# Optimization experiments

Hardware: AMD Instinct MI355X
Metric: run time of the kernel (lower is better)

The kernel has to match this reference:

```python
import jax, jax.numpy as jnp
import numpy as np

B, T, SD, DD = 256, 365, 64, 16
H, NH, L, FF = 256, 8, 4, 1024
K, P, N = 5, 30, 10000
DEG = np.pi / 180.0


def _ln(x, g, b):
    mu = x.mean(-1, keepdims=True)
    var = ((x - mu) ** 2).mean(-1, keepdims=True)
    return g * (x - mu) / jnp.sqrt(var + 1e-5) + b


def _gelu(x):
    return jax.nn.gelu(x, approximate=False)


def _forward(static, dynamic, lat, lon, all_statics, station_coords,
             W_st, b_st, g_st, be_st, W_dy, b_dy, g_dy, be_dy,
             Wqkv, bqkv, Wo, bo, g_ln1, be_ln1, Wf1, bf1, Wf2, bf2, g_ln2, be_ln2,
             W_o1, b_o1, W_o2, b_o2, scale, shift):
    # denormalize to CONUS degrees, then radians (as BallTree haversine expects)
    lat_o = (lat + 1.0) / 2.0 * (49.0 - 24.0) + 24.0
    lon_o = (lon + 1.0) / 2.0 * (-66.5 + 125.0) - 125.0
    qlat = lat_o[:, 0] * DEG
    qlon = lon_o[:, 0] * DEG
    slat = station_coords[:, 0]
    slon = station_coords[:, 1]
    dlat = qlat[:, None] - slat[None, :]
    dlon = qlon[:, None] - slon[None, :]
    # haversine term; true distance = 2*asin(sqrt(hav)) is monotone in hav,
    # so ranking by hav reproduces BallTree(metric='haversine') neighbor order
    hav = jnp.sin(dlat / 2) ** 2 + jnp.cos(qlat)[:, None] * jnp.cos(slat)[None, :] * jnp.sin(dlon / 2) ** 2
    _, nbr = jax.lax.top_k(-hav, K + 1)          # [B, K+1] nearest stations
    nbr = nbr[:, 1:]                              # drop self (nearest), keep K
    neigh = all_statics[nbr].reshape(static.shape[0], K * SD)  # gather + flatten
    combined = jnp.concatenate([static, neigh], axis=-1)       # [B, (K+1)*SD]

    sfeat = _gelu(_ln(combined @ W_st + b_st, g_st, be_st))    # static_net (dropout=eval)
    x = _gelu(_ln(dynamic @ W_dy + b_dy, g_dy, be_dy)) + sfeat[:, None, :]

    hd = H // NH
    inv_sqrt_d = 1.0 / jnp.sqrt(jnp.float32(hd))
    Bq, Tq = x.shape[0], x.shape[1]
    for l in range(L):  # post-norm TransformerEncoderLayer, relu FF
        qkv = x @ Wqkv[l] + bqkv[l]
        q, k, v = jnp.split(qkv, 3, axis=-1)
        q = q.reshape(Bq, Tq, NH, hd)
        k = k.reshape(Bq, Tq, NH, hd)
        v = v.reshape(Bq, Tq, NH, hd)
        att = jax.nn.softmax(jnp.einsum('bqhd,bkhd->bhqk', q, k) * inv_sqrt_d, axis=-1)
        ao = jnp.einsum('bhqk,bkhd->bqhd', att, v).reshape(Bq, Tq, H) @ Wo[l] + bo[l]
        x = _ln(x + ao, g_ln1[l], be_ln1[l])
        ff = jax.nn.relu(x @ Wf1[l] + bf1[l]) @ Wf2[l] + bf2[l]
        x = _ln(x + ff, g_ln2[l], be_ln2[l])

    pooled = x.mean(axis=1)
    raw = jnp.tanh(_gelu((pooled + sfeat) @ W_o1 + b_o1) @ W_o2 + b_o2)
    return raw * scale + shift


def setup_inputs() -> dict:
    key = jax.random.key(0)
    ks = jax.random.split(key, 24)
    rn = lambda k, shp: jax.random.normal(k, shp, jnp.float32) * 0.02
    inp = {}
    inp['static'] = jax.random.normal(ks[0], (B, SD), jnp.float32)
    inp['dynamic'] = jax.random.normal(ks[1], (B, T, DD), jnp.float32)
    inp['lat'] = jax.random.uniform(ks[2], (B, 1), jnp.float32, -1.0, 1.0)
    inp['lon'] = jax.random.uniform(ks[3], (B, 1), jnp.float32, -1.0, 1.0)
    inp['all_statics'] = jax.random.normal(ks[4], (N, SD), jnp.float32)
    slat = jax.random.uniform(ks[5], (N,), jnp.float32, 24.0, 49.0) * DEG
    slon = jax.random.uniform(ks[6], (N,), jnp.float32, -125.0, -66.5) * DEG
    inp['station_coords'] = jnp.stack([slat, slon], axis=-1)
    # static_net
    inp['W_st'] = rn(ks[7], (SD * (K + 1), H)); inp['b_st'] = jnp.zeros(H)
    inp['g_st'] = jnp.ones(H); inp['be_st'] = jnp.zeros(H)
    # dynamic_emb
    inp['W_dy'] = rn(ks[8], (DD, H)); inp['b_dy'] = jnp.zeros(H)
    inp['g_dy'] = jnp.ones(H); inp['be_dy'] = jnp.zeros(H)
    # transformer (stacked over layers)
    inp['Wqkv'] = rn(ks[9], (L, H, 3 * H)); inp['bqkv'] = jnp.zeros((L, 3 * H))
    inp['Wo'] = rn(ks[10], (L, H, H)); inp['bo'] = jnp.zeros((L, H))
    inp['g_ln1'] = jnp.ones((L, H)); inp['be_ln1'] = jnp.zeros((L, H))
    inp['Wf1'] = rn(ks[11], (L, H, FF)); inp['bf1'] = jnp.zeros((L, FF))
    inp['Wf2'] = rn(ks[12], (L, FF, H)); inp['bf2'] = jnp.zeros((L, H))
    inp['g_ln2'] = jnp.ones((L, H)); inp['be_ln2'] = jnp.zeros((L, H))
    # output head
    inp['W_o1'] = rn(ks[13], (H, H // 2)); inp['b_o1'] = jnp.zeros(H // 2)
    inp['W_o2'] = rn(ks[14], (H // 2, P)); inp['b_o2'] = jnp.zeros(P)
    inp['scale'] = jnp.array(1.0, jnp.float32)
    inp['shift'] = jnp.array(0.0, jnp.float32)
    return inp


def reference(static, dynamic, lat, lon, all_statics, station_coords,
              W_st, b_st, g_st, be_st, W_dy, b_dy, g_dy, be_dy,
              Wqkv, bqkv, Wo, bo, g_ln1, be_ln1, Wf1, bf1, Wf2, bf2, g_ln2, be_ln2,
              W_o1, b_o1, W_o2, b_o2, scale, shift):
    return _forward(static, dynamic, lat, lon, all_statics, station_coords,
                    W_st, b_st, g_st, be_st, W_dy, b_dy, g_dy, be_dy,
                    Wqkv, bqkv, Wo, bo, g_ln1, be_ln1, Wf1, bf1, Wf2, bf2, g_ln2, be_ln2,
                    W_o1, b_o1, W_o2, b_o2, scale, shift)
```

## Files before the change

kernel.cpp:

```cpp
#include <hip/hip_runtime.h>
#include <math.h>

#define T_SEQ 365
#define HDIM 256
#define NHEADS 8
#define HD 32
#define BATCH 256
#define DDIM 16
#define FFDIM 1024
#define NST 10000
#define KNB 5
#define SDIM 64

typedef __bf16 bf16x8 __attribute__((ext_vector_type(8)));
typedef float  f32x16 __attribute__((ext_vector_type(16)));
typedef unsigned short u16x8 __attribute__((ext_vector_type(8)));

__device__ __forceinline__ ushort f2b_hi(float v) {
    unsigned u = __float_as_uint(v);
    unsigned r = u + 0x7fffu + ((u >> 16) & 1u);
    return (ushort)(r >> 16);
}
__device__ __forceinline__ float b2f(ushort h) {
    return __uint_as_float(((unsigned)h) << 16);
}
__device__ __forceinline__ ushort f2b_lo(float v, ushort hi) {
    return f2b_hi(v - b2f(hi));
}

__device__ __forceinline__ float gelu_f(float x) {
    return 0.5f * x * (1.f + erff(x * 0.70710678118654752f));
}


__device__ __forceinline__ float block_sum256(float v, float* sred) {
    #pragma unroll
    for (int off = 32; off; off >>= 1) v += __shfl_xor(v, off);
    int wave = threadIdx.x >> 6;
    if ((threadIdx.x & 63) == 0) sred[wave] = v;
    __syncthreads();
    float s = sred[0] + sred[1] + sred[2] + sred[3];
    __syncthreads();
    return s;
}

__global__ __launch_bounds__(256) void topk_kernel(
    const float* __restrict__ lat, const float* __restrict__ lon,
    const float* __restrict__ coords, int* __restrict__ nbr)
{
    __shared__ float hav[NST];
    __shared__ float rv[256];
    __shared__ int   ri[256];
    const float DEG = 0.017453292519943295f;
    int b = blockIdx.x, t = threadIdx.x;
    float lat_o = (lat[b] + 1.f) * 0.5f * 25.f + 24.f;
    float lon_o = (lon[b] + 1.f) * 0.5f * 58.5f - 125.f;
    float qlat = lat_o * DEG, qlon = lon_o * DEG;
    float cq = cosf(qlat);
    for (int i = t; i < NST; i += 256) {
        float slat = coords[2*i], slon = coords[2*i+1];
        float dlat = qlat - slat, dlon = qlon - slon;
        float s1 = sinf(dlat * 0.5f), s2 = sinf(dlon * 0.5f);
        hav[i] = s1*s1 + cq * cosf(slat) * s2*s2;
    }
    __syncthreads();
    for (int sel = 0; sel < KNB + 1; ++sel) {
        float bv = 1e30f; int bi = 0x7fffffff;
        for (int i = t; i < NST; i += 256) {
            float v = hav[i];
            if (v < bv || (v == bv && i < bi)) { bv = v; bi = i; }
        }
        rv[t] = bv; ri[t] = bi;
        __syncthreads();
        for (int s = 128; s > 0; s >>= 1) {
            if (t < s) {
                float ov = rv[t+s]; int oi = ri[t+s];
                if (ov < rv[t] || (ov == rv[t] && oi < ri[t])) { rv[t] = ov; ri[t] = oi; }
            }
            __syncthreads();
        }
        if (t == 0) {
            if (sel > 0) nbr[b*KNB + sel - 1] = ri[0];
            hav[ri[0]] = 1e30f;
        }
        __syncthreads();
    }
}

__global__ __launch_bounds__(256) void sfeat_kernel(
    const float* __restrict__ stat, const float* __restrict__ all_st,
    const int* __restrict__ nbr, const float* __restrict__ W,
    const float* __restrict__ bias, const float* __restrict__ g,
    const float* __restrict__ be, float* __restrict__ sfeat)
{
    __shared__ float comb[(KNB+1)*SDIM];
    __shared__ float sred[4];
    int b = blockIdx.x, t = threadIdx.x;
    for (int i = t; i < (KNB+1)*SDIM; i += 256) {
        if (i < SDIM) comb[i] = stat[b*SDIM + i];
        else {
            int n = (i - SDIM) >> 6, d = (i - SDIM) & 63;
            comb[i] = all_st[(size_t)nbr[b*KNB + n] * SDIM + d];
        }
    }
    __syncthreads();
    float acc = bias[t];
    for (int j = 0; j < (KNB+1)*SDIM; ++j)
        acc = fmaf(comb[j], W[j*HDIM + t], acc);
    float mu  = block_sum256(acc, sred) * (1.f/256.f);
    float d   = acc - mu;
    float var = block_sum256(d*d, sred) * (1.f/256.f);
    float y = g[t] * d * rsqrtf(var + 1e-5f) + be[t];
    sfeat[(size_t)b*HDIM + t] = gelu_f(y);
}

__global__ __launch_bounds__(256) void dyn_kernel(
    const float* __restrict__ dynv, const float* __restrict__ W,
    const float* __restrict__ bias, const float* __restrict__ g,
    const float* __restrict__ be, const float* __restrict__ sfeatc,
    ushort* __restrict__ xhi, ushort* __restrict__ xlo)
{
    __shared__ float w[DDIM*HDIM];
    __shared__ float dr[4][DDIM];
    int wave = threadIdx.x >> 6, lane = threadIdx.x & 63;
    int row0 = blockIdx.x * 4;
    for (int i = threadIdx.x; i < DDIM*HDIM; i += 256) w[i] = W[i];
    if (lane < DDIM)
        dr[wave][lane] = dynv[(size_t)(row0 + wave)*DDIM + lane];
    __syncthreads();
    int row = row0 + wave;
    int b = row / T_SEQ;
    int c0 = lane * 4;
    float v0 = bias[c0], v1 = bias[c0+1], v2 = bias[c0+2], v3 = bias[c0+3];
    #pragma unroll
    for (int k = 0; k < DDIM; ++k) {
        float dk = dr[wave][k];
        float4 wv = *reinterpret_cast<const float4*>(&w[k*HDIM + c0]);
        v0 = fmaf(dk, wv.x, v0); v1 = fmaf(dk, wv.y, v1);
        v2 = fmaf(dk, wv.z, v2); v3 = fmaf(dk, wv.w, v3);
    }
    float s = v0 + v1 + v2 + v3;
    #pragma unroll
    for (int off = 32; off; off >>= 1) s += __shfl_xor(s, off);
    float mu = s * (1.f/256.f);
    float d0 = v0-mu, d1 = v1-mu, d2 = v2-mu, d3 = v3-mu;
    float s2 = d0*d0 + d1*d1 + d2*d2 + d3*d3;
    #pragma unroll
    for (int off = 32; off; off >>= 1) s2 += __shfl_xor(s2, off);
    float rs = rsqrtf(s2 * (1.f/256.f) + 1e-5f);
    float4 gg = *reinterpret_cast<const float4*>(&g[c0]);
    float4 bb = *reinterpret_cast<const float4*>(&be[c0]);
    float4 sf = *reinterpret_cast<const float4*>(&sfeatc[(size_t)b*HDIM + c0]);
    float o0 = gelu_f(gg.x*d0*rs + bb.x) + sf.x;
    float o1 = gelu_f(gg.y*d1*rs + bb.y) + sf.y;
    float o2 = gelu_f(gg.z*d2*rs + bb.z) + sf.z;
    float o3 = gelu_f(gg.w*d3*rs + bb.w) + sf.w;
    size_t o = ((size_t)(row >> 5) * 32 + (c0 >> 3)) * 256 + ((row & 31) << 3) + (c0 & 7);
    ushort4 hv, lv;
    hv.x = f2b_hi(o0); lv.x = f2b_lo(o0, hv.x);
    hv.y = f2b_hi(o1); lv.y = f2b_lo(o1, hv.y);
    hv.z = f2b_hi(o2); lv.z = f2b_lo(o2, hv.z);
    hv.w = f2b_hi(o3); lv.w = f2b_lo(o3, hv.w);
    *reinterpret_cast<ushort4*>(&xhi[o]) = hv;
    *reinterpret_cast<ushort4*>(&xlo[o]) = lv;
}

__global__ __launch_bounds__(256) void tsplit_kernel(
    const float* __restrict__ W, ushort* __restrict__ hi, ushort* __restrict__ lo,
    int K, int N)
{
    __shared__ float tile[32][33];
    size_t l = blockIdx.z;
    const float* Wl = W + l*(size_t)K*N;
    ushort* hil = hi + l*(size_t)K*N;
    ushort* lol = lo + l*(size_t)K*N;
    int n0 = blockIdx.x*32, k0 = blockIdx.y*32;
    int tx = threadIdx.x & 31, ty = threadIdx.x >> 5;
    int KB = K >> 3;
    for (int i = ty; i < 32; i += 8) tile[i][tx] = Wl[(size_t)(k0+i)*N + n0 + tx];
    __syncthreads();
    for (int i = ty; i < 32; i += 8) {
        float v = tile[tx][i];
        ushort h = f2b_hi(v);
        size_t o = ((size_t)(n0 >> 5) * KB + (k0 >> 3) + (tx >> 3)) * 256
                 + ((size_t)i << 3) + (tx & 7);
        hil[o] = h;
        lol[o] = f2b_lo(v, h);
    }
}

template<int DO_RELU, int OUT>
__global__ __launch_bounds__(256) void gemm_mfma(
    const ushort* __restrict__ Ahi, const ushort* __restrict__ Alo,
    const ushort* __restrict__ Bhi, const ushort* __restrict__ Blo,
    const float* __restrict__ bias,
    ushort* __restrict__ Chi, ushort* __restrict__ Clo,
    ushort* __restrict__ Wq_h, ushort* __restrict__ Wq_l,
    ushort* __restrict__ Wk_h, ushort* __restrict__ Wk_l,
    ushort* __restrict__ Wv_h, ushort* __restrict__ Wv_l,
    int M, int N, int K)
{
    const int t = threadIdx.x;
    const int lane = t & 63, wave = t >> 6;
    const int wr = wave >> 1, wc = wave & 1;
    const int lr = lane & 31, kg = lane >> 5;
    const int row_b = blockIdx.y * 128 + wr * 64;
    const int col_b = blockIdx.x * 128 + wc * 64;
    const int KB = K >> 3;

    const ushort *pAh[2], *pAl[2], *pBh[2], *pBl[2];
    #pragma unroll
    for (int mi = 0; mi < 2; ++mi) {
        int rb = row_b + mi*32; if (rb > M - 32) rb = M - 32;
        size_t base = ((size_t)(rb >> 5) * KB + kg) * 256 + lr * 8;
        pAh[mi] = Ahi + base; pAl[mi] = Alo + base;
    }
    #pragma unroll
    for (int nj = 0; nj < 2; ++nj) {
        size_t base = ((size_t)((col_b + nj*32) >> 5) * KB + kg) * 256 + lr * 8;
        pBh[nj] = Bhi + base; pBl[nj] = Blo + base;
    }

    f32x16 acc[2][2];
    #pragma unroll
    for (int i = 0; i < 2; ++i)
        #pragma unroll
        for (int j = 0; j < 2; ++j)
            #pragma unroll
            for (int r = 0; r < 16; ++r) acc[i][j][r] = 0.f;

    bf16x8 a0h[2], a0l[2], b0h[2], b0l[2];
    bf16x8 a1h[2], a1l[2], b1h[2], b1l[2];

#define LOADF(AH, AL, BH, BL, OFF) do {                                        \
    _Pragma("unroll") for (int mi = 0; mi < 2; ++mi) {                         \
        AH[mi] = *reinterpret_cast<const bf16x8*>(pAh[mi] + (OFF));            \
        AL[mi] = *reinterpret_cast<const bf16x8*>(pAl[mi] + (OFF)); }          \
    _Pragma("unroll") for (int nj = 0; nj < 2; ++nj) {                         \
        BH[nj] = *reinterpret_cast<const bf16x8*>(pBh[nj] + (OFF));            \
        BL[nj] = *reinterpret_cast<const bf16x8*>(pBl[nj] + (OFF)); } } while(0)

#define MFMAF(AH, AL, BH, BL) do {                                             \
    _Pragma("unroll") for (int mi = 0; mi < 2; ++mi)                           \
    _Pragma("unroll") for (int nj = 0; nj < 2; ++nj) {                         \
        acc[mi][nj] = __builtin_amdgcn_mfma_f32_32x32x16_bf16(                 \
            AH[mi], BH[nj], acc[mi][nj], 0, 0, 0);                             \
        acc[mi][nj] = __builtin_amdgcn_mfma_f32_32x32x16_bf16(                 \
            AH[mi], BL[nj], acc[mi][nj], 0, 0, 0);                             \
        acc[mi][nj] = __builtin_amdgcn_mfma_f32_32x32x16_bf16(                 \
            AL[mi], BH[nj], acc[mi][nj], 0, 0, 0); } } while(0)

    LOADF(a0h, a0l, b0h, b0l, 0);
    for (int k0 = 0; k0 < K; k0 += 32) {
        size_t o1 = (size_t)((k0 + 16) >> 3) * 256;
        LOADF(a1h, a1l, b1h, b1l, o1);
        MFMAF(a0h, a0l, b0h, b0l);
        size_t o2 = (k0 + 32 < K) ? (size_t)((k0 + 32) >> 3) * 256 : 0;
        LOADF(a0h, a0l, b0h, b0l, o2);
        MFMAF(a1h, a1l, b1h, b1l);
    }
#undef LOADF
#undef MFMAF

    #pragma unroll
    for (int mi = 0; mi < 2; ++mi) {
        int rb2 = row_b + mi*32;
        #pragma unroll
        for (int nj = 0; nj < 2; ++nj) {
            int colf = col_b + nj*32 + lr;
            float bv = bias[colf];
            if (OUT == 1) {
                size_t ftb = ((size_t)(rb2 >> 5) * (N >> 3) + (colf >> 3)) * 256 + (colf & 7);
                #pragma unroll
                for (int r = 0; r < 16; ++r) {
                    int r31 = (r & 3) + 8*(r >> 2) + 4*kg;
                    int row = rb2 + r31;
                    if (row >= M) continue;
                    float v = acc[mi][nj][r] + bv;
                    if (DO_RELU) v = fmaxf(v, 0.f);
                    size_t oo = ftb + (size_t)r31 * 8;
                    ushort hh = f2b_hi(v);
                    Chi[oo] = hh;
                    Clo[oo] = f2b_lo(v, hh);
                }
            } else {
                int sel = (col_b + nj*32) >> 8;
                int h = (colf >> 5) & 7;
                int d = colf & 31;
                #pragma unroll
                for (int r = 0; r < 16; ++r) {
                    int r31 = (r & 3) + 8*(r >> 2) + 4*kg;
                    int row = rb2 + r31;
                    if (row >= M) continue;
                    float v = acc[mi][nj][r] + bv;
                    int bl = row / T_SEQ;
                    int tok = row - bl * T_SEQ;
                    size_t bb = (size_t)(bl*8 + h) * 12288;
                    ushort hh = f2b_hi(v);
                    ushort ll = f2b_lo(v, hh);
                    if (sel == 0) {
                        size_t o = bb + (size_t)((tok >> 5)*4 + (d >> 3))*256
                                 + ((tok & 31) << 3) + (d & 7);
                        Wq_h[o] = hh; Wq_l[o] = ll;
                    } else if (sel == 1) {
                        size_t o = bb + (size_t)((tok >> 5)*4 + (d >> 3))*256
                                 + ((tok & 31) << 3) + (d & 7);
                        Wk_h[o] = hh; Wk_l[o] = ll;
                    } else {
                        size_t o = bb + (size_t)(tok >> 3)*256 + d*8 + (tok & 7);
                        Wv_h[o] = hh; Wv_l[o] = ll;
                    }
                }
            }
        }
    }
}

__global__ __launch_bounds__(256) void gemm_ln(
    const ushort* __restrict__ Ahi, const ushort* __restrict__ Alo,
    const ushort* __restrict__ Bhi, const ushort* __restrict__ Blo,
    const float* __restrict__ bias,
    ushort* __restrict__ xhi, ushort* __restrict__ xlo,
    const float* __restrict__ g, const float* __restrict__ be,
    int M, int K)
{
    const int N = HDIM;
    const int t = threadIdx.x;
    const int lane = t & 63, wave = t >> 6;
    const int lr = lane & 31, kg = lane >> 5;
    const int row_b = blockIdx.y * 32;
    const int col_w = wave * 64;
    const int KB = K >> 3;

    const ushort *pAh, *pAl, *pBh[2], *pBl[2];
    {
        size_t base = ((size_t)(row_b >> 5) * KB + kg) * 256 + lr * 8;
        pAh = Ahi + base; pAl = Alo + base;
    }
    #pragma unroll
    for (int nj = 0; nj < 2; ++nj) {
        size_t base = ((size_t)((col_w + nj*32) >> 5) * KB + kg) * 256 + lr * 8;
        pBh[nj] = Bhi + base; pBl[nj] = Blo + base;
    }

    f32x16 acc[2];
    #pragma unroll
    for (int j = 0; j < 2; ++j)
        #pragma unroll
        for (int r = 0; r < 16; ++r) acc[j][r] = 0.f;

    bf16x8 a0h, a0l, b0h[2], b0l[2];
    bf16x8 a1h, a1l, b1h[2], b1l[2];

#define LOADF(AH, AL, BH, BL, OFF) do {                                        \
    AH = *reinterpret_cast<const bf16x8*>(pAh + (OFF));                        \
    AL = *reinterpret_cast<const bf16x8*>(pAl + (OFF));                        \
    _Pragma("unroll") for (int nj = 0; nj < 2; ++nj) {                         \
        BH[nj] = *reinterpret_cast<const bf16x8*>(pBh[nj] + (OFF));            \
        BL[nj] = *reinterpret_cast<const bf16x8*>(pBl[nj] + (OFF)); } } while(0)

#define MFMAF(AH, AL, BH, BL) do {                                             \
    _Pragma("unroll") for (int nj = 0; nj < 2; ++nj) {                         \
        acc[nj] = __builtin_amdgcn_mfma_f32_32x32x16_bf16(                     \
            AH, BH[nj], acc[nj], 0, 0, 0);                                     \
        acc[nj] = __builtin_amdgcn_mfma_f32_32x32x16_bf16(                     \
            AH, BL[nj], acc[nj], 0, 0, 0);                                     \
        acc[nj] = __builtin_amdgcn_mfma_f32_32x32x16_bf16(                     \
            AL, BH[nj], acc[nj], 0, 0, 0); } } while(0)

    LOADF(a0h, a0l, b0h, b0l, 0);
    for (int k0 = 0; k0 < K; k0 += 32) {
        size_t o1 = (size_t)((k0 + 16) >> 3) * 256;
        LOADF(a1h, a1l, b1h, b1l, o1);
        MFMAF(a0h, a0l, b0h, b0l);
        size_t o2 = (k0 + 32 < K) ? (size_t)((k0 + 32) >> 3) * 256 : 0;
        LOADF(a0h, a0l, b0h, b0l, o2);
        MFMAF(a1h, a1l, b1h, b1l);
    }
#undef LOADF
#undef MFMAF

    float s1[16], s2[16];
    #pragma unroll
    for (int nj = 0; nj < 2; ++nj) {
        int col = col_w + nj*32 + lr;
        float bv = bias[col];
        #pragma unroll
        for (int r = 0; r < 16; ++r) {
            int r31 = (r & 3) + 8*(r >> 2) + 4*kg;
            int row = row_b + r31;
            size_t oo = ((size_t)(row >> 5) * (N >> 3) + (col >> 3)) * 256
                      + ((row & 31) << 3) + (col & 7);
            float v = acc[nj][r] + bv + b2f(xhi[oo]) + b2f(xlo[oo]);
            acc[nj][r] = v;
            if (nj == 0) { s1[r] = v;  s2[r] = v*v; }
            else         { s1[r] += v; s2[r] += v*v; }
        }
    }
    #pragma unroll
    for (int r = 0; r < 16; ++r) {
        #pragma unroll
        for (int off = 1; off <= 16; off <<= 1) {
            s1[r] += __shfl_xor(s1[r], off);
            s2[r] += __shfl_xor(s2[r], off);
        }
    }
    __shared__ float red1[4][32];
    __shared__ float red2[4][32];
    __shared__ float tot1[32];
    __shared__ float tot2[32];
    if (lr == 0) {
        #pragma unroll
        for (int r = 0; r < 16; ++r) {
            int rr = (r & 3) + 8*(r >> 2) + 4*kg;
            red1[wave][rr] = s1[r];
            red2[wave][rr] = s2[r];
        }
    }
    __syncthreads();
    if (t < 32) {
        tot1[t] = red1[0][t] + red1[1][t] + red1[2][t] + red1[3][t];
        tot2[t] = red2[0][t] + red2[1][t] + red2[2][t] + red2[3][t];
    }
    __syncthreads();
    #pragma unroll
    for (int r = 0; r < 16; ++r) {
        int r31 = (r & 3) + 8*(r >> 2) + 4*kg;
        int row = row_b + r31;
        float mu = tot1[r31] * (1.f/256.f);
        float var = fmaf(-mu, mu, tot2[r31] * (1.f/256.f));
        float rs = rsqrtf(var + 1e-5f);
        #pragma unroll
        for (int nj = 0; nj < 2; ++nj) {
            int col = col_w + nj*32 + lr;
            float o = g[col] * (acc[nj][r] - mu) * rs + be[col];
            size_t oo = ((size_t)(row >> 5) * (N >> 3) + (col >> 3)) * 256
                      + ((row & 31) << 3) + (col & 7);
            ushort hh = f2b_hi(o);
            xhi[oo] = hh;
            xlo[oo] = f2b_lo(o, hh);
        }
    }
}

__global__ __launch_bounds__(256) void attn_mfma(
    const ushort* __restrict__ Qh, const ushort* __restrict__ Ql,
    const ushort* __restrict__ Kh, const ushort* __restrict__ Kl,
    const ushort* __restrict__ Vh, const ushort* __restrict__ Vl,
    ushort* __restrict__ ahi, ushort* __restrict__ alo)
{
    const int bh = blockIdx.y;
    const int wave = threadIdx.x >> 6, lane = threadIdx.x & 63;
    const int qt = blockIdx.x * 4 + wave;
    const int lr = lane & 31, kg = lane >> 5;
    const size_t base = (size_t)bh * 12288;
    const float scale = 0.17677669529663687f;

    bf16x8 qfh[2], qfl[2];
    #pragma unroll
    for (int ks = 0; ks < 2; ++ks) {
        size_t o = base + (size_t)(qt*4 + ks*2 + kg)*256 + lr*8;
        qfh[ks] = *reinterpret_cast<const bf16x8*>(Qh + o);
        qfl[ks] = *reinterpret_cast<const bf16x8*>(Ql + o);
    }

    float m = -3e38f, l = 0.f;
    f32x16 oacc;
    #pragma unroll
    for (int r = 0; r < 16; ++r) oacc[r] = 0.f;

    for (int kt = 0; kt < 12; ++kt) {
        f32x16 st;
        #pragma unroll
        for (int r = 0; r < 16; ++r) st[r] = 0.f;
        #pragma unroll
        for (int ks = 0; ks < 2; ++ks) {
            size_t o = base + (size_t)(kt*4 + ks*2 + kg)*256 + lr*8;
            bf16x8 kfh = *reinterpret_cast<const bf16x8*>(Kh + o);
            bf16x8 kfl = *reinterpret_cast<const bf16x8*>(Kl + o);
            st = __builtin_amdgcn_mfma_f32_32x32x16_bf16(kfh, qfh[ks], st, 0,0,0);
            st = __builtin_amdgcn_mfma_f32_32x32x16_bf16(kfh, qfl[ks], st, 0,0,0);
            st = __builtin_amdgcn_mfma_f32_32x32x16_bf16(kfl, qfh[ks], st, 0,0,0);
        }
        float p[16];
        float tm = -3e38f;
        #pragma unroll
        for (int r = 0; r < 16; ++r) {
            int krow = kt*32 + (r & 3) + 8*(r >> 2) + 4*kg;
            p[r] = (krow < T_SEQ) ? st[r] : -3e38f;
            tm = fmaxf(tm, p[r]);
        }
        tm = fmaxf(tm, __shfl_xor(tm, 32));
        float newm = fmaxf(m, tm);
        float f = __expf((m - newm) * scale);
        m = newm;
        l *= f;
        float sumL = 0.f;
        #pragma unroll
        for (int r = 0; r < 16; ++r) {
            float e = __expf((p[r] - m) * scale);
            p[r] = e; sumL += e;
        }
        l += sumL;
        #pragma unroll
        for (int r = 0; r < 16; ++r) {
            int r31 = (r & 3) + 8*(r >> 2) + 4*kg;
            float fr = __shfl(f, r31);
            oacc[r] *= fr;
        }
        float pp[16];
        #pragma unroll
        for (int r = 0; r < 16; ++r) pp[r] = __shfl_xor(p[r], 32);
        #pragma unroll
        for (int ks = 0; ks < 2; ++ks) {
            union { u16x8 u; bf16x8 b; } fh, fl;
            #pragma unroll
            for (int j = 0; j < 8; ++j) {
                float e;
                if (ks == 0)
                    e = kg ? ((j < 4) ? pp[4+j] : p[j])
                           : ((j < 4) ? p[j]    : pp[j-4]);
                else
                    e = kg ? ((j < 4) ? pp[12+j] : p[8+j])
                           : ((j < 4) ? p[8+j]   : pp[4+j]);
                ushort hh = f2b_hi(e);
                fh.u[j] = hh;
                fl.u[j] = f2b_lo(e, hh);
            }
            size_t vo = base + (size_t)(kt*4 + ks*2 + kg)*256 + lr*8;
            bf16x8 vfh = *reinterpret_cast<const bf16x8*>(Vh + vo);
            bf16x8 vfl = *reinterpret_cast<const bf16x8*>(Vl + vo);
            oacc = __builtin_amdgcn_mfma_f32_32x32x16_bf16(fh.b, vfh, oacc, 0,0,0);
            oacc = __builtin_amdgcn_mfma_f32_32x32x16_bf16(fh.b, vfl, oacc, 0,0,0);
            oacc = __builtin_amdgcn_mfma_f32_32x32x16_bf16(fl.b, vfh, oacc, 0,0,0);
        }
    }
    l += __shfl_xor(l, 32);
    float il = 1.f / l;

    const int bl = bh >> 3, h = bh & 7;
    #pragma unroll
    for (int r = 0; r < 16; ++r) {
        int q = (r & 3) + 8*(r >> 2) + 4*kg;
        float sc = __shfl(il, q);
        int row_local = qt*32 + q;
        if (row_local < T_SEQ) {
            float v = oacc[r] * sc;
            int grow = bl*T_SEQ + row_local;
            int col = h*32 + lr;
            size_t o = ((size_t)(grow >> 5)*32 + (col >> 3))*256
                     + ((grow & 31) << 3) + (col & 7);
            ushort hh = f2b_hi(v);
            ahi[o] = hh;
            alo[o] = f2b_lo(v, hh);
        }
    }
}

__global__ __launch_bounds__(256) void pool_kernel(
    const ushort* __restrict__ xhi, const ushort* __restrict__ xlo,
    float* __restrict__ pooled)
{
    int b = blockIdx.x, t = threadIdx.x;
    float acc = 0.f;
    for (int tt = 0; tt < T_SEQ; ++tt) {
        size_t row = (size_t)b*T_SEQ + tt;
        size_t o = ((row >> 5) * 32 + (t >> 3)) * 256 + ((row & 31) << 3) + (t & 7);
        acc += b2f(xhi[o]) + b2f(xlo[o]);
    }
    pooled[(size_t)b*HDIM + t] = acc * (1.f/365.f);
}

__global__ __launch_bounds__(256) void head_kernel(
    const float* __restrict__ pooled, const float* __restrict__ sfeat,
    const float* __restrict__ W1, const float* __restrict__ b1,
    const float* __restrict__ W2, const float* __restrict__ b2,
    const float* __restrict__ scale, const float* __restrict__ shift,
    float* __restrict__ out)
{
    __shared__ float p[HDIM];
    __shared__ float h1[HDIM/2];
    int b = blockIdx.x, t = threadIdx.x;
    p[t] = pooled[(size_t)b*HDIM + t] + sfeat[(size_t)b*HDIM + t];
    __syncthreads();
    if (t < HDIM/2) {
        float a = b1[t];
        for (int c = 0; c < HDIM; ++c) a = fmaf(p[c], W1[c*(HDIM/2) + t], a);
        h1[t] = gelu_f(a);
    }
    __syncthreads();
    if (t < 30) {
        float a = b2[t];
        for (int j = 0; j < HDIM/2; ++j) a = fmaf(h1[j], W2[j*30 + t], a);
        out[b*30 + t] = tanhf(a) * scale[0] + shift[0];
    }
}

extern "C" void kernel_launch(void* const* d_in, const int* in_sizes, int n_in,
                              void* d_out, int out_size, void* d_ws, size_t ws_size,
                              hipStream_t stream) {
    const float* p_static = (const float*)d_in[0];
    const float* p_dyn    = (const float*)d_in[1];
    const float* p_lat    = (const float*)d_in[2];
    const float* p_lon    = (const float*)d_in[3];
    const float* p_all    = (const float*)d_in[4];
    const float* p_coords = (const float*)d_in[5];
    const float* p_Wst    = (const float*)d_in[6];
    const float* p_bst    = (const float*)d_in[7];
    const float* p_gst    = (const float*)d_in[8];
    const float* p_best   = (const float*)d_in[9];
    const float* p_Wdy    = (const float*)d_in[10];
    const float* p_bdy    = (const float*)d_in[11];
    const float* p_gdy    = (const float*)d_in[12];
    const float* p_bedy   = (const float*)d_in[13];
    const float* p_Wqkv   = (const float*)d_in[14];
    const float* p_bqkv   = (const float*)d_in[15];
    const float* p_Wo     = (const float*)d_in[16];
    const float* p_bo     = (const float*)d_in[17];
    const float* p_gln1   = (const float*)d_in[18];
    const float* p_beln1  = (const float*)d_in[19];
    const float* p_Wf1    = (const float*)d_in[20];
    const float* p_bf1    = (const float*)d_in[21];
    const float* p_Wf2    = (const float*)d_in[22];
    const float* p_bf2    = (const float*)d_in[23];
    const float* p_gln2   = (const float*)d_in[24];
    const float* p_beln2  = (const float*)d_in[25];
    const float* p_Wo1    = (const float*)d_in[26];
    const float* p_bo1    = (const float*)d_in[27];
    const float* p_Wo2    = (const float*)d_in[28];
    const float* p_bo2    = (const float*)d_in[29];
    const float* p_scale  = (const float*)d_in[30];
    const float* p_shift  = (const float*)d_in[31];
    float* out = (float*)d_out;
    (void)in_sizes; (void)n_in; (void)out_size;

    char* ws = (char*)d_ws;
    size_t off = 0;
    auto alloc = [&](size_t bytes) -> void* {
        void* p = ws + off;
        off += (bytes + 255) & ~(size_t)255;
        return p;
    };
    int*    nbr    = (int*)   alloc((size_t)BATCH*KNB*sizeof(int));
    float*  sfeat  = (float*) alloc((size_t)BATCH*HDIM*sizeof(float));
    float*  pooled = (float*) alloc((size_t)BATCH*HDIM*sizeof(float));
    const size_t SZ_QKV = (size_t)4*768*256, SZ_O = (size_t)4*256*256;
    const size_t SZ_F1  = (size_t)4*1024*256, SZ_F2 = (size_t)4*256*1024;
    ushort* Wqkvt_h = (ushort*)alloc(SZ_QKV*2*sizeof(ushort)); ushort* Wqkvt_l = Wqkvt_h + SZ_QKV;
    ushort* Wot_h   = (ushort*)alloc(SZ_O  *2*sizeof(ushort)); ushort* Wot_l   = Wot_h   + SZ_O;
    ushort* Wf1t_h  = (ushort*)alloc(SZ_F1 *2*sizeof(ushort)); ushort* Wf1t_l  = Wf1t_h  + SZ_F1;
    ushort* Wf2t_h  = (ushort*)alloc(SZ_F2 *2*sizeof(ushort)); ushort* Wf2t_l  = Wf2t_h  + SZ_F2;
    size_t fixed = off;

    const size_t X_CH   = (size_t)T_SEQ * HDIM * 4;
    const size_t REG_CH = (size_t)1553408;
    const size_t PER_CH = X_CH + REG_CH;
    int CH = 32;
    {
        const int tiers[3] = {256, 128, 64};
        for (int i = 0; i < 3; ++i) {
            if (fixed + (size_t)tiers[i]*PER_CH + 8192 <= ws_size) { CH = tiers[i]; break; }
        }
    }
    const int RW = CH * T_SEQ;
    ushort* xh  = (ushort*)alloc((size_t)CH * X_CH);
    ushort* xl  = xh + (size_t)RW * HDIM;
    char*   big = (char*)alloc((size_t)CH * REG_CH);
    const size_t seg = (size_t)CH * 8 * 12288;
    ushort* Qh  = (ushort*)big;
    ushort* Ql  = Qh  + seg;
    ushort* Kh2 = Ql  + seg;
    ushort* Kl2 = Kh2 + seg;
    ushort* Vth = Kl2 + seg;
    ushort* Vtl = Vth + seg;
    ushort* aatt_h = Vtl + seg;
    ushort* aatt_l = aatt_h + (size_t)RW * HDIM;
    ushort* hbuf_h = (ushort*)big;
    ushort* hbuf_l = hbuf_h + (size_t)RW * FFDIM;
    const int GY  = (RW + 127) / 128;
    const int GY3 = RW / 32;

    topk_kernel <<<BATCH, 256, 0, stream>>>(p_lat, p_lon, p_coords, nbr);
    sfeat_kernel<<<BATCH, 256, 0, stream>>>(p_static, p_all, nbr, p_Wst, p_bst, p_gst, p_best, sfeat);
    tsplit_kernel<<<dim3(24, 8, 4), 256, 0, stream>>>(p_Wqkv, Wqkvt_h, Wqkvt_l, 256, 768);
    tsplit_kernel<<<dim3( 8, 8, 4), 256, 0, stream>>>(p_Wo,   Wot_h,   Wot_l,   256, 256);
    tsplit_kernel<<<dim3(32, 8, 4), 256, 0, stream>>>(p_Wf1,  Wf1t_h,  Wf1t_l,  256, 1024);
    tsplit_kernel<<<dim3( 8,32, 4), 256, 0, stream>>>(p_Wf2,  Wf2t_h,  Wf2t_l,  1024, 256);

    const int NCHUNK = BATCH / CH;
    for (int c = 0; c < NCHUNK; ++c) {
        dyn_kernel<<<RW/4, 256, 0, stream>>>(
            p_dyn + (size_t)c*CH*T_SEQ*DDIM, p_Wdy, p_bdy, p_gdy, p_bedy,
            sfeat + (size_t)c*CH*HDIM, xh, xl);
        for (int l = 0; l < 4; ++l) {
            gemm_mfma<0,2><<<dim3(6, GY), 256, 0, stream>>>(
                xh, xl, Wqkvt_h + (size_t)l*768*256, Wqkvt_l + (size_t)l*768*256,
                p_bqkv + l*768, nullptr, nullptr,
                Qh, Ql, Kh2, Kl2, Vth, Vtl, RW, 768, 256);
            attn_mfma<<<dim3(3, CH*8), 256, 0, stream>>>(
                Qh, Ql, Kh2, Kl2, Vth, Vtl, aatt_h, aatt_l);
            gemm_ln<<<dim3(1, GY3), 256, 0, stream>>>(
                aatt_h, aatt_l, Wot_h + (size_t)l*256*256, Wot_l + (size_t)l*256*256,
                p_bo + l*256, xh, xl, p_gln1 + l*256, p_beln1 + l*256, RW, 256);
            gemm_mfma<1,1><<<dim3(8, GY), 256, 0, stream>>>(
                xh, xl, Wf1t_h + (size_t)l*1024*256, Wf1t_l + (size_t)l*1024*256,
                p_bf1 + l*1024, hbuf_h, hbuf_l,
                nullptr, nullptr, nullptr, nullptr, nullptr, nullptr, RW, 1024, 256);
            gemm_ln<<<dim3(1, GY3), 256, 0, stream>>>(
                hbuf_h, hbuf_l, Wf2t_h + (size_t)l*256*1024, Wf2t_l + (size_t)l*256*1024,
                p_bf2 + l*256, xh, xl, p_gln2 + l*256, p_beln2 + l*256, RW, 1024);
        }
        pool_kernel<<<CH, 256, 0, stream>>>(xh, xl, pooled + (size_t)c*CH*HDIM);
    }
    head_kernel<<<BATCH, 256, 0, stream>>>(pooled, sfeat, p_Wo1, p_bo1, p_Wo2, p_bo2, p_scale, p_shift, out);
}
```

Baseline: 4.584 ms.

## Fuse feed-forward GEMMs with residual LayerNorm and remap workgroups for XCD locality

Replaces the two FF kernels (FF1 GEMM writing a 1024-wide hidden buffer, then FF2 GEMM with LayerNorm) with one kernel. Each wave computes a 32-row hidden tile in registers, converts it to split bf16 hi/lo, and accumulates FF2 directly before residual add and LayerNorm. This removes the write and re-read of the large hidden buffer. The cost is heavy register use (eight 32x32 accumulators per wave), weights streamed from global without LDS sharing, and few waves per CU. It also swizzles workgroup IDs in the QKV GEMM for XCD-friendly scheduling and swaps the attention grid dimensions so blocks of the same head are adjacent.

```diff
diff --git a/kernel.cpp b/kernel.cpp
--- a/kernel.cpp
+++ b/kernel.cpp
@@ -189,12 +189,10 @@
     }
 }
 
-template<int DO_RELU, int OUT>
-__global__ __launch_bounds__(256) void gemm_mfma(
+__global__ __launch_bounds__(256) void gemm_qkv(
     const ushort* __restrict__ Ahi, const ushort* __restrict__ Alo,
     const ushort* __restrict__ Bhi, const ushort* __restrict__ Blo,
     const float* __restrict__ bias,
-    ushort* __restrict__ Chi, ushort* __restrict__ Clo,
     ushort* __restrict__ Wq_h, ushort* __restrict__ Wq_l,
     ushort* __restrict__ Wk_h, ushort* __restrict__ Wk_l,
     ushort* __restrict__ Wv_h, ushort* __restrict__ Wv_l,
@@ -204,8 +202,14 @@
     const int lane = t & 63, wave = t >> 6;
     const int wr = wave >> 1, wc = wave & 1;
     const int lr = lane & 31, kg = lane >> 5;
-    const int row_b = blockIdx.y * 128 + wr * 64;
-    const int col_b = blockIdx.x * 128 + wc * 64;
+    int nwg = gridDim.x * gridDim.y;
+    int orig = blockIdx.y * gridDim.x + blockIdx.x;
+    int qq = nwg >> 3, rr = nwg & 7, xcd = orig & 7, idx = orig >> 3;
+    int wgid = (xcd < rr ? xcd*(qq+1) : rr*(qq+1) + (xcd-rr)*qq) + idx;
+    const int bx = wgid % gridDim.x;
+    const int by = wgid / gridDim.x;
+    const int row_b = by * 128 + wr * 64;
+    const int col_b = bx * 128 + wc * 64;
     const int KB = K >> 3;
 
     const ushort *pAh[2], *pAl[2], *pBh[2], *pBl[2];
@@ -269,47 +273,31 @@
         for (int nj = 0; nj < 2; ++nj) {
             int colf = col_b + nj*32 + lr;
             float bv = bias[colf];
-            if (OUT == 1) {
-                size_t ftb = ((size_t)(rb2 >> 5) * (N >> 3) + (colf >> 3)) * 256 + (colf & 7);
-                #pragma unroll
-                for (int r = 0; r < 16; ++r) {
-                    int r31 = (r & 3) + 8*(r >> 2) + 4*kg;
-                    int row = rb2 + r31;
-                    if (row >= M) continue;
-                    float v = acc[mi][nj][r] + bv;
-                    if (DO_RELU) v = fmaxf(v, 0.f);
-                    size_t oo = ftb + (size_t)r31 * 8;
-                    ushort hh = f2b_hi(v);
-                    Chi[oo] = hh;
-                    Clo[oo] = f2b_lo(v, hh);
-                }
-            } else {
-                int sel = (col_b + nj*32) >> 8;
-                int h = (colf >> 5) & 7;
-                int d = colf & 31;
-                #pragma unroll
-                for (int r = 0; r < 16; ++r) {
-                    int r31 = (r & 3) + 8*(r >> 2) + 4*kg;
-                    int row = rb2 + r31;
-                    if (row >= M) continue;
-                    float v = acc[mi][nj][r] + bv;
-                    int bl = row / T_SEQ;
-                    int tok = row - bl * T_SEQ;
-                    size_t bb = (size_t)(bl*8 + h) * 12288;
-                    ushort hh = f2b_hi(v);
-                    ushort ll = f2b_lo(v, hh);
-                    if (sel == 0) {
-                        size_t o = bb + (size_t)((tok >> 5)*4 + (d >> 3))*256
-                                 + ((tok & 31) << 3) + (d & 7);
-                        Wq_h[o] = hh; Wq_l[o] = ll;
-                    } else if (sel == 1) {
-                        size_t o = bb + (size_t)((tok >> 5)*4 + (d >> 3))*256
-                                 + ((tok & 31) << 3) + (d & 7);
-                        Wk_h[o] = hh; Wk_l[o] = ll;
-                    } else {
-                        size_t o = bb + (size_t)(tok >> 3)*256 + d*8 + (tok & 7);
-                        Wv_h[o] = hh; Wv_l[o] = ll;
-                    }
+            int sel = (col_b + nj*32) >> 8;
+            int h = (colf >> 5) & 7;
+            int d = colf & 31;
+            #pragma unroll
+            for (int r = 0; r < 16; ++r) {
+                int r31 = (r & 3) + 8*(r >> 2) + 4*kg;
+                int row = rb2 + r31;
+                if (row >= M) continue;
+                float v = acc[mi][nj][r] + bv;
+                int bl = row / T_SEQ;
+                int tok = row - bl * T_SEQ;
+                size_t bb = (size_t)(bl*8 + h) * 12288;
+                ushort hh = f2b_hi(v);
+                ushort ll = f2b_lo(v, hh);
+                if (sel == 0) {
+                    size_t o = bb + (size_t)((tok >> 5)*4 + (d >> 3))*256
+                             + ((tok & 31) << 3) + (d & 7);
+                    Wq_h[o] = hh; Wq_l[o] = ll;
+                } else if (sel == 1) {
+                    size_t o = bb + (size_t)((tok >> 5)*4 + (d >> 3))*256
+                             + ((tok & 31) << 3) + (d & 7);
+                    Wk_h[o] = hh; Wk_l[o] = ll;
+                } else {
+                    size_t o = bb + (size_t)(tok >> 3)*256 + d*8 + (tok & 7);
+                    Wv_h[o] = hh; Wv_l[o] = ll;
                 }
             }
         }
@@ -443,15 +431,133 @@
     }
 }
 
+__global__ __launch_bounds__(256) void ff_fused(
+    const ushort* __restrict__ W1h, const ushort* __restrict__ W1l,
+    const ushort* __restrict__ W2h, const ushort* __restrict__ W2l,
+    const float* __restrict__ b1, const float* __restrict__ b2,
+    ushort* __restrict__ xhi, ushort* __restrict__ xlo,
+    const float* __restrict__ g, const float* __restrict__ be,
+    int M)
+{
+    const int lane = threadIdx.x & 63, wave = threadIdx.x >> 6;
+    const int lr = lane & 31, kg = lane >> 5;
+    const int row_b = (blockIdx.x * 4 + wave) * 32;
+    if (row_b >= M) return;
+
+    const size_t xbase = ((size_t)(row_b >> 5) * 32) * 256 + lr * 8;
+
+    f32x16 oacc[8];
+    #pragma unroll
+    for (int ct = 0; ct < 8; ++ct)
+        #pragma unroll
+        for (int r = 0; r < 16; ++r) oacc[ct][r] = 0.f;
+
+    for (int nt = 0; nt < 32; ++nt) {
+        f32x16 st;
+        #pragma unroll
+        for (int r = 0; r < 16; ++r) st[r] = 0.f;
+        #pragma unroll
+        for (int ks = 0; ks < 16; ++ks) {
+            size_t wo = ((size_t)nt * 32 + ks * 2 + kg) * 256 + lr * 8;
+            bf16x8 wh = *reinterpret_cast<const bf16x8*>(W1h + wo);
+            bf16x8 wl = *reinterpret_cast<const bf16x8*>(W1l + wo);
+            size_t xo = xbase + (size_t)(ks * 2 + kg) * 256;
+            bf16x8 xh8 = *reinterpret_cast<const bf16x8*>(xhi + xo);
+            bf16x8 xl8 = *reinterpret_cast<const bf16x8*>(xlo + xo);
+            st = __builtin_amdgcn_mfma_f32_32x32x16_bf16(wh, xh8, st, 0,0,0);
+            st = __builtin_amdgcn_mfma_f32_32x32x16_bf16(wh, xl8, st, 0,0,0);
+            st = __builtin_amdgcn_mfma_f32_32x32x16_bf16(wl, xh8, st, 0,0,0);
+        }
+        float p[16];
+        #pragma unroll
+        for (int r = 0; r < 16; ++r) {
+            int n = nt*32 + (r & 3) + 8*(r >> 2) + 4*kg;
+            p[r] = fmaxf(st[r] + b1[n], 0.f);
+        }
+        float pp[16];
+        #pragma unroll
+        for (int r = 0; r < 16; ++r) pp[r] = __shfl_xor(p[r], 32);
+        #pragma unroll
+        for (int ks = 0; ks < 2; ++ks) {
+            union { u16x8 u; bf16x8 b; } fh, fl;
+            #pragma unroll
+            for (int j = 0; j < 8; ++j) {
+                float e;
+                if (ks == 0)
+                    e = kg ? ((j < 4) ? pp[4+j] : p[j])
+                           : ((j < 4) ? p[j]    : pp[j-4]);
+                else
+                    e = kg ? ((j < 4) ? pp[12+j] : p[8+j])
+                           : ((j < 4) ? p[8+j]   : pp[4+j]);
+                ushort hh = f2b_hi(e);
+                fh.u[j] = hh;
+                fl.u[j] = f2b_lo(e, hh);
+            }
+            #pragma unroll
+            for (int ct = 0; ct < 8; ++ct) {
+                size_t wo = ((size_t)ct * 128 + nt * 4 + ks * 2 + kg) * 256 + lr * 8;
+                bf16x8 wh = *reinterpret_cast<const bf16x8*>(W2h + wo);
+                bf16x8 wl = *reinterpret_cast<const bf16x8*>(W2l + wo);
+                oacc[ct] = __builtin_amdgcn_mfma_f32_32x32x16_bf16(fh.b, wh, oacc[ct], 0,0,0);
+                oacc[ct] = __builtin_amdgcn_mfma_f32_32x32x16_bf16(fh.b, wl, oacc[ct], 0,0,0);
+                oacc[ct] = __builtin_amdgcn_mfma_f32_32x32x16_bf16(fl.b, wh, oacc[ct], 0,0,0);
+            }
+        }
+    }
+    float s1[16], s2[16];
+    #pragma unroll
+    for (int ct = 0; ct < 8; ++ct) {
+        int col = ct*32 + lr;
+        float bv = b2[col];
+        #pragma unroll
+        for (int r = 0; r < 16; ++r) {
+            int r31 = (r & 3) + 8*(r >> 2) + 4*kg;
+            int row = row_b + r31;
+            size_t oo = ((size_t)(row >> 5) * 32 + (col >> 3)) * 256
+                      + ((row & 31) << 3) + (col & 7);
+            float v = oacc[ct][r] + bv + b2f(xhi[oo]) + b2f(xlo[oo]);
+            oacc[ct][r] = v;
+            if (ct == 0) { s1[r] = v;  s2[r] = v*v; }
+            else         { s1[r] += v; s2[r] += v*v; }
+        }
+    }
+    #pragma unroll
+    for (int r = 0; r < 16; ++r) {
+        #pragma unroll
+        for (int off = 1; off <= 16; off <<= 1) {
+            s1[r] += __shfl_xor(s1[r], off);
+            s2[r] += __shfl_xor(s2[r], off);
+        }
+    }
+    #pragma unroll
+    for (int r = 0; r < 16; ++r) {
+        int r31 = (r & 3) + 8*(r >> 2) + 4*kg;
+        int row = row_b + r31;
+        float mu = s1[r] * (1.f/256.f);
+        float var = fmaf(-mu, mu, s2[r] * (1.f/256.f));
+        float rs = rsqrtf(var + 1e-5f);
+        #pragma unroll
+        for (int ct = 0; ct < 8; ++ct) {
+            int col = ct*32 + lr;
+            float o = g[col] * (oacc[ct][r] - mu) * rs + be[col];
+            size_t oo = ((size_t)(row >> 5) * 32 + (col >> 3)) * 256
+                      + ((row & 31) << 3) + (col & 7);
+            ushort hh = f2b_hi(o);
+            xhi[oo] = hh;
+            xlo[oo] = f2b_lo(o, hh);
+        }
+    }
+}
+
 __global__ __launch_bounds__(256) void attn_mfma(
     const ushort* __restrict__ Qh, const ushort* __restrict__ Ql,
     const ushort* __restrict__ Kh, const ushort* __restrict__ Kl,
     const ushort* __restrict__ Vh, const ushort* __restrict__ Vl,
     ushort* __restrict__ ahi, ushort* __restrict__ alo)
 {
-    const int bh = blockIdx.y;
+    const int bh = blockIdx.x;
     const int wave = threadIdx.x >> 6, lane = threadIdx.x & 63;
-    const int qt = blockIdx.x * 4 + wave;
+    const int qt = blockIdx.y * 4 + wave;
     const int lr = lane & 31, kg = lane >> 5;
     const size_t base = (size_t)bh * 12288;
     const float scale = 0.17677669529663687f;
@@ -675,10 +781,9 @@
     ushort* Vtl = Vth + seg;
     ushort* aatt_h = Vtl + seg;
     ushort* aatt_l = aatt_h + (size_t)RW * HDIM;
-    ushort* hbuf_h = (ushort*)big;
-    ushort* hbuf_l = hbuf_h + (size_t)RW * FFDIM;
     const int GY  = (RW + 127) / 128;
     const int GY3 = RW / 32;
+    const int GFF = (RW/32 + 3) / 4;
 
     topk_kernel <<<BATCH, 256, 0, stream>>>(p_lat, p_lon, p_coords, nbr);
     sfeat_kernel<<<BATCH, 256, 0, stream>>>(p_static, p_all, nbr, p_Wst, p_bst, p_gst, p_best, sfeat);
@@ -693,22 +798,20 @@
             p_dyn + (size_t)c*CH*T_SEQ*DDIM, p_Wdy, p_bdy, p_gdy, p_bedy,
             sfeat + (size_t)c*CH*HDIM, xh, xl);
         for (int l = 0; l < 4; ++l) {
-            gemm_mfma<0,2><<<dim3(6, GY), 256, 0, stream>>>(
+            gemm_qkv<<<dim3(6, GY), 256, 0, stream>>>(
                 xh, xl, Wqkvt_h + (size_t)l*768*256, Wqkvt_l + (size_t)l*768*256,
-                p_bqkv + l*768, nullptr, nullptr,
+                p_bqkv + l*768,
                 Qh, Ql, Kh2, Kl2, Vth, Vtl, RW, 768, 256);
-            attn_mfma<<<dim3(3, CH*8), 256, 0, stream>>>(
+            attn_mfma<<<dim3(CH*8, 3), 256, 0, stream>>>(
                 Qh, Ql, Kh2, Kl2, Vth, Vtl, aatt_h, aatt_l);
             gemm_ln<<<dim3(1, GY3), 256, 0, stream>>>(
                 aatt_h, aatt_l, Wot_h + (size_t)l*256*256, Wot_l + (size_t)l*256*256,
                 p_bo + l*256, xh, xl, p_gln1 + l*256, p_beln1 + l*256, RW, 256);
-            gemm_mfma<1,1><<<dim3(8, GY), 256, 0, stream>>>(
-                xh, xl, Wf1t_h + (size_t)l*1024*256, Wf1t_l + (size_t)l*1024*256,
-                p_bf1 + l*1024, hbuf_h, hbuf_l,
-                nullptr, nullptr, nullptr, nullptr, nullptr, nullptr, RW, 1024, 256);
-            gemm_ln<<<dim3(1, GY3), 256, 0, stream>>>(
-                hbuf_h, hbuf_l, Wf2t_h + (size_t)l*256*1024, Wf2t_l + (size_t)l*256*1024,
-                p_bf2 + l*256, xh, xl, p_gln2 + l*256, p_beln2 + l*256, RW, 1024);
+            ff_fused<<<GFF, 256, 0, stream>>>(
+                Wf1t_h + (size_t)l*1024*256, Wf1t_l + (size_t)l*1024*256,
+                Wf2t_h + (size_t)l*256*1024, Wf2t_l + (size_t)l*256*1024,
+                p_bf1 + l*1024, p_bf2 + l*256,
+                xh, xl, p_gln2 + l*256, p_beln2 + l*256, RW);
         }
         pool_kernel<<<CH, 256, 0, stream>>>(xh, xl, pooled + (size_t)c*CH*HDIM);
     }
```

After: 10.24 ms. 123% more time.
